# Kernel optimization log

Hardware: AMD Instinct MI355X
Metric: run time of the kernel (lower is better)

Reference implementation:

```python
import jax, jax.numpy as jnp
import numpy as np

B, N, D, H, I = 16, 1024, 1024, 16, 4096
HS = D // H  # 64
EPS = 1e-5


def setup_inputs() -> dict:
    key = jax.random.key(0)
    ks = jax.random.split(key, 8)
    w = lambda k, shape: (jax.random.normal(k, shape, jnp.float32) * 0.02)
    return {
        'hidden_states': jax.random.normal(ks[0], (B, N, D), jnp.float32),
        'ln1_g': jnp.ones((D,), jnp.float32), 'ln1_b': jnp.zeros((D,), jnp.float32),
        'ln2_g': jnp.ones((D,), jnp.float32), 'ln2_b': jnp.zeros((D,), jnp.float32),
        'wq': w(ks[1], (D, D)), 'bq': jnp.zeros((D,), jnp.float32),
        'wk': w(ks[2], (D, D)), 'bk': jnp.zeros((D,), jnp.float32),
        'wv': w(ks[3], (D, D)), 'bv': jnp.zeros((D,), jnp.float32),
        'w1': w(ks[4], (D, I)), 'b1': jnp.zeros((I,), jnp.float32),
        'w2': w(ks[5], (I, D)), 'b2': jnp.zeros((D,), jnp.float32),
    }


def _layernorm(x, g, b):
    m = jnp.mean(x, axis=-1, keepdims=True)
    v = jnp.var(x, axis=-1, keepdims=True)
    return (x - m) * jax.lax.rsqrt(v + EPS) * g + b


def _split_heads(t):
    # Faithful to transpose_for_scores: reshape (B,N,HS,H) -> (B,H,N,HS)
    # i.e. head h takes the strided feature slice t[..., h::H].
    b, n, _ = t.shape
    return t.reshape(b, n, HS, H).transpose(0, 3, 1, 2)


def _vit_layer(x, ln1_g, ln1_b, ln2_g, ln2_b, wq, bq, wk, bk, wv, bv, w1, b1, w2, b2):
    h = _layernorm(x, ln1_g, ln1_b)
    q = _split_heads(h @ wq + bq)  # [B,H,N,HS]
    k = _split_heads(h @ wk + bk)
    v = _split_heads(h @ wv + bv)
    scores = jax.nn.softmax(jnp.einsum('bhqd,bhkd->bhqk', q, k) / np.sqrt(HS).astype(np.float32), axis=-1)
    attn = jnp.einsum('bhqk,bhkd->bhqd', scores, v)          # [B,H,N,HS]
    attn = attn.transpose(0, 2, 1, 3).reshape(x.shape)       # head-major merge (as in source)
    x = x + attn
    h = _layernorm(x, ln2_g, ln2_b)
    mlp = jax.nn.silu(h @ w1 + b1) @ w2 + b2
    return x + mlp


def reference(hidden_states, ln1_g, ln1_b, ln2_g, ln2_b, wq, bq, wk, bk, wv, bv, w1, b1, w2, b2):
    return _vit_layer(hidden_states, ln1_g, ln1_b, ln2_g, ln2_b, wq, bq, wk, bk, wv, bv, w1, b1, w2, b2)
```

## Files before the change

### kernel.cpp

```cpp
#include <hip/hip_runtime.h>
#include <hip/hip_bf16.h>
#include <stdint.h>

typedef __bf16 bf16;
typedef bf16 bf16x8 __attribute__((ext_vector_type(8)));
typedef bf16 bf16x4 __attribute__((ext_vector_type(4)));
typedef float f32x4 __attribute__((ext_vector_type(4)));

static __device__ __forceinline__ f32x4 mfma16(bf16x8 a, bf16x8 b, f32x4 c) {
    return __builtin_amdgcn_mfma_f32_16x16x32_bf16(a, b, c, 0, 0, 0);
}

static __device__ __forceinline__ void gld16(const bf16* g, bf16* l) {
    __builtin_amdgcn_global_load_lds((const __attribute__((address_space(1))) void*)g,
                                     (__attribute__((address_space(3))) void*)l, 16, 0, 0);
}

static __device__ __forceinline__ uint32_t pkbf(float a, float b) {
    union { bf16 h[2]; uint32_t u; } u_;
    u_.h[0] = (bf16)a; u_.h[1] = (bf16)b;
    return u_.u;
}

template <int PERM>
__global__ __launch_bounds__(256)
void tcast_kernel(const float* __restrict__ src, bf16* __restrict__ dst, int R, int C) {
    __shared__ float t[32][33];
    const int tx = threadIdx.x, ty = threadIdx.y;
    const int c0 = blockIdx.x * 32, r0 = blockIdx.y * 32;
#pragma unroll
    for (int j = 0; j < 4; ++j)
        t[ty + j * 8][tx] = src[(size_t)(r0 + ty + j * 8) * C + c0 + tx];
    __syncthreads();
#pragma unroll
    for (int j = 0; j < 4; ++j) {
        const int c = c0 + ty + j * 8;
        const int cp = PERM ? (((c & 15) << 6) | (c >> 4)) : c;
        dst[(size_t)cp * R + r0 + tx] = (bf16)t[tx][ty + j * 8];
    }
}

__global__ __launch_bounds__(256)
void bperm_kernel(const float* __restrict__ b0, const float* __restrict__ b1,
                  const float* __restrict__ b2, float* __restrict__ dst) {
    const int i = blockIdx.x * 256 + threadIdx.x;
    const int seg = i >> 10, c = i & 1023;
    const int src = ((c & 63) << 4) | (c >> 6);
    const float* b = (seg == 0) ? b0 : (seg == 1) ? b1 : b2;
    dst[i] = b[src];
}

__global__ __launch_bounds__(256)
void ln_kernel(const float* __restrict__ x, const float* __restrict__ gg,
               const float* __restrict__ bb, bf16* __restrict__ out) {
    __shared__ float red[8];
    const int row = blockIdx.x, tid = threadIdx.x;
    const int lane = tid & 63, wid = tid >> 6;
    const float4 v = ((const float4*)(x + (size_t)row * 1024))[tid];
    float s  = v.x + v.y + v.z + v.w;
    float s2 = v.x * v.x + v.y * v.y + v.z * v.z + v.w * v.w;
#pragma unroll
    for (int m = 1; m <= 32; m <<= 1) {
        s  += __shfl_xor(s,  m);
        s2 += __shfl_xor(s2, m);
    }
    if (lane == 0) { red[wid] = s; red[wid + 4] = s2; }
    __syncthreads();
    float ts  = red[0] + red[1] + red[2] + red[3];
    float ts2 = red[4] + red[5] + red[6] + red[7];
    float mean = ts * (1.f / 1024.f);
    float var  = ts2 * (1.f / 1024.f) - mean * mean;
    float rs   = rsqrtf(var + 1e-5f);
    const float4 gv = ((const float4*)gg)[tid];
    const float4 bv = ((const float4*)bb)[tid];
    bf16x4 o;
    o[0] = (bf16)((v.x - mean) * rs * gv.x + bv.x);
    o[1] = (bf16)((v.y - mean) * rs * gv.y + bv.y);
    o[2] = (bf16)((v.z - mean) * rs * gv.z + bv.z);
    o[3] = (bf16)((v.w - mean) * rs * gv.w + bv.w);
    *(bf16x4*)(out + (size_t)row * 1024 + tid * 4) = o;
}

template <int MODE>
__global__ __launch_bounds__(256)
void gemm_bt(const bf16* __restrict__ A, const bf16* __restrict__ Bt,
             int M, int N, int K,
             const float* __restrict__ bias_a,
             const float* __restrict__ resid, float* __restrict__ outF,
             bf16* __restrict__ oQ, bf16* __restrict__ oK, bf16* __restrict__ oV,
             bf16* __restrict__ oB) {
    __shared__ alignas(16) bf16 As[3][128 * 32];
    __shared__ alignas(16) bf16 Bs[3][128 * 32];
    const int tid = threadIdx.x;
    const int wid = tid >> 6, lane = tid & 63;
    const int li = lane & 15, g = lane >> 4;

    const int nwg = gridDim.x * gridDim.y;
    const int orig = blockIdx.y * gridDim.x + blockIdx.x;
    const int wg = (orig & 7) * (nwg >> 3) + (orig >> 3);
    const int bx = wg % gridDim.x, by = wg / gridDim.x;

    const int row0 = by * 128, col0 = bx * 128;

    const int gsrc = ((tid & 3) ^ ((tid >> 3) & 3)) * 8;
    const bf16* gA0 = A + (size_t)(row0 + (tid >> 2)) * K + gsrc;
    const bf16* gA1 = A + (size_t)(row0 + 64 + (tid >> 2)) * K + gsrc;
    const bf16* gB0 = Bt + (size_t)(col0 + (tid >> 2)) * K + gsrc;
    const bf16* gB1 = Bt + (size_t)(col0 + 64 + (tid >> 2)) * K + gsrc;

    const int wr = wid >> 1, wc = wid & 1;
    f32x4 acc[4][4] = {};

    const int nt = K >> 5;
#pragma unroll
    for (int p = 0; p < 2; ++p) {
        const int kk = p << 5;
        gld16(gA0 + kk, &As[p][wid * 512]);
        gld16(gA1 + kk, &As[p][wid * 512 + 2048]);
        gld16(gB0 + kk, &Bs[p][wid * 512]);
        gld16(gB1 + kk, &Bs[p][wid * 512 + 2048]);
    }

    const int sa = (li >> 1) & 3;
    const int rdoff = (g ^ sa) * 8;

    int cur = 0;
    for (int t = 0; t < nt; ++t) {
        if (t + 2 < nt) {
            const int k2 = (t + 2) << 5;
            const int nb = (cur + 2) % 3;
            gld16(gA0 + k2, &As[nb][wid * 512]);
            gld16(gA1 + k2, &As[nb][wid * 512 + 2048]);
            gld16(gB0 + k2, &Bs[nb][wid * 512]);
            gld16(gB1 + k2, &Bs[nb][wid * 512 + 2048]);
            asm volatile("s_waitcnt vmcnt(8)" ::: "memory");
        } else if (t + 1 < nt) {
            asm volatile("s_waitcnt vmcnt(4)" ::: "memory");
        } else {
            asm volatile("s_waitcnt vmcnt(0)" ::: "memory");
        }
        __builtin_amdgcn_s_barrier();
        __builtin_amdgcn_sched_barrier(0);

        bf16x8 af[4], bg[4];
        const bf16* pa = &As[cur][(wr * 64 + li) * 32 + rdoff];
        const bf16* pb = &Bs[cur][(wc * 64 + li) * 32 + rdoff];
#pragma unroll
        for (int i = 0; i < 4; ++i) af[i] = *(const bf16x8*)(pa + i * 512);
#pragma unroll
        for (int j = 0; j < 4; ++j) bg[j] = *(const bf16x8*)(pb + j * 512);
#pragma unroll
        for (int i = 0; i < 4; ++i)
#pragma unroll
            for (int j = 0; j < 4; ++j)
                acc[i][j] = mfma16(af[i], bg[j], acc[i][j]);
        __builtin_amdgcn_sched_barrier(0);
        __builtin_amdgcn_s_barrier();
        cur = (cur + 1) % 3;
    }

    if (MODE == 0) {
        const int seg = col0 >> 10;
        const int h   = ((col0 & 1023) >> 6) + wc;
        const int bb  = row0 >> 10;
        const int n0  = (row0 & 1023) + wr * 64;
        float bias[4];
#pragma unroll
        for (int j = 0; j < 4; ++j) bias[j] = bias_a[col0 + wc * 64 + j * 16 + li];

        if (seg == 2) {
#pragma unroll
            for (int i = 0; i < 4; ++i)
#pragma unroll
                for (int j = 0; j < 4; ++j) {
                    const int d = j * 16 + li;
                    bf16x4 pv;
#pragma unroll
                    for (int r = 0; r < 4; ++r) pv[r] = (bf16)(acc[i][j][r] + bias[j]);
                    *(bf16x4*)(oV + ((size_t)(bb * 16 + h) * 64 + d) * 1024
                                   + n0 + i * 16 + g * 4) = pv;
                }
        } else {
            char* ep = (wid < 3) ? ((char*)&As[0][0] + wid * 8192)
                                 : ((char*)&Bs[0][0]);
            const float scale = (seg == 0) ? 0.125f : 1.0f;
            bf16* og = (seg == 0) ? oQ : oK;
#pragma unroll
            for (int i = 0; i < 4; ++i)
#pragma unroll
                for (int j = 0; j < 4; ++j)
#pragma unroll
                    for (int r = 0; r < 4; ++r) {
                        const int rr = i * 16 + g * 4 + r;
                        const int byte = (rr * 128 + (j * 16 + li) * 2) ^ ((rr & 7) << 4);
                        *(bf16*)(ep + byte) = (bf16)((acc[i][j][r] + bias[j]) * scale);
                    }
            bf16* gb = og + ((size_t)(bb * 16 + h) * 1024 + n0) * 64;
#pragma unroll
            for (int t = 0; t < 8; ++t) {
                const int rr = t * 8 + (lane >> 3);
                const int d0 = (lane & 7) * 8;
                const int byte = (rr * 128 + d0 * 2) ^ ((rr & 7) << 4);
                bf16x8 val = *(const bf16x8*)(ep + byte);
                *(bf16x8*)(gb + (size_t)rr * 64 + d0) = val;
            }
        }
    } else {
#pragma unroll
        for (int i = 0; i < 4; ++i) {
            const int row = row0 + wr * 64 + i * 16 + g * 4;
#pragma unroll
            for (int j = 0; j < 4; ++j) {
                const int col = col0 + wc * 64 + j * 16 + li;
                f32x4 v = acc[i][j];
                if (MODE == 1) {
                    const float bias = bias_a[col];
#pragma unroll
                    for (int r = 0; r < 4; ++r) {
                        float val = v[r] + bias;
                        val = val / (1.f + __expf(-val));
                        oB[(size_t)(row + r) * N + col] = (bf16)val;
                    }
                } else {
                    const float bias = bias_a[col];
#pragma unroll
                    for (int r = 0; r < 4; ++r) {
                        const size_t idx = (size_t)(row + r) * N + col;
                        outF[idx] = v[r] + bias + resid[idx];
                    }
                }
            }
        }
    }
}

template <int MODE>
__global__ __launch_bounds__(512, 2)
void gemm256(const bf16* __restrict__ A, const bf16* __restrict__ Bt,
             int M, int N, int K,
             const float* __restrict__ bias_a,
             const float* __restrict__ resid, float* __restrict__ outF,
             bf16* __restrict__ oB) {
    __shared__ alignas(16) bf16 As[2][256 * 64];
    __shared__ alignas(16) bf16 Bs[2][256 * 64];
    const int tid = threadIdx.x;
    const int wid = tid >> 6, lane = tid & 63;
    const int li = lane & 15, g = lane >> 4;
    const int wm = wid >> 2, wn = wid & 3;

    const int nwg = gridDim.x * gridDim.y;
    const int orig = blockIdx.y * gridDim.x + blockIdx.x;
    const int wg = (orig & 7) * (nwg >> 3) + (orig >> 3);
    const int bx = wg % gridDim.x, by = wg / gridDim.x;
    const int row0 = by * 256, col0 = bx * 256;

    const int gsrc = ((tid & 7) ^ ((tid >> 3) & 7)) << 3;
    const bf16* gA = A + (size_t)(row0 + (tid >> 3)) * K + gsrc;
    const bf16* gB = Bt + (size_t)(col0 + (tid >> 3)) * K + gsrc;

    f32x4 acc[8][4] = {};
    const int nt = K >> 6;

#pragma unroll
    for (int j = 0; j < 4; ++j) {
        gld16(gA + (size_t)(64 * j) * K, &As[0][j * 4096 + (wid << 9)]);
        gld16(gB + (size_t)(64 * j) * K, &Bs[0][j * 4096 + (wid << 9)]);
    }

    int cur = 0;
    for (int t = 0; t < nt; ++t) {
        if (t + 1 < nt) {
            const size_t koff = (size_t)(t + 1) << 6;
#pragma unroll
            for (int j = 0; j < 4; ++j) {
                gld16(gA + (size_t)(64 * j) * K + koff, &As[cur ^ 1][j * 4096 + (wid << 9)]);
                gld16(gB + (size_t)(64 * j) * K + koff, &Bs[cur ^ 1][j * 4096 + (wid << 9)]);
            }
            asm volatile("s_waitcnt vmcnt(8)" ::: "memory");
        } else {
            asm volatile("s_waitcnt vmcnt(0)" ::: "memory");
        }
        __builtin_amdgcn_s_barrier();
        __builtin_amdgcn_sched_barrier(0);

        const bf16* At = &As[cur][0];
        const bf16* Bl = &Bs[cur][0];
        bf16x8 bfr[4][2];
#pragma unroll
        for (int p = 0; p < 4; ++p) {
            bf16x8 af[2][2];
#pragma unroll
            for (int ii = 0; ii < 2; ++ii) {
                const int rr = wm * 128 + (p * 2 + ii) * 16 + li;
#pragma unroll
                for (int ks = 0; ks < 2; ++ks)
                    af[ii][ks] = *(const bf16x8*)(At + rr * 64 + (((ks * 4 + g) ^ (li & 7)) << 3));
            }
            if (p == 0) {
#pragma unroll
                for (int jf = 0; jf < 4; ++jf) {
                    const int rb = wn * 64 + jf * 16 + li;
#pragma unroll
                    for (int ks = 0; ks < 2; ++ks)
                        bfr[jf][ks] = *(const bf16x8*)(Bl + rb * 64 + (((ks * 4 + g) ^ (li & 7)) << 3));
                }
            }
            asm volatile("s_waitcnt lgkmcnt(0)" ::: "memory");
            __builtin_amdgcn_sched_barrier(0);
            __builtin_amdgcn_s_setprio(1);
#pragma unroll
            for (int ii = 0; ii < 2; ++ii)
#pragma unroll
                for (int jf = 0; jf < 4; ++jf)
#pragma unroll
                    for (int ks = 0; ks < 2; ++ks)
                        acc[p * 2 + ii][jf] = mfma16(af[ii][ks], bfr[jf][ks], acc[p * 2 + ii][jf]);
            __builtin_amdgcn_s_setprio(0);
            __builtin_amdgcn_sched_barrier(0);
            __builtin_amdgcn_s_barrier();
        }
        cur ^= 1;
    }

#pragma unroll
    for (int i = 0; i < 8; ++i) {
        const int row = row0 + wm * 128 + i * 16 + g * 4;
#pragma unroll
        for (int jf = 0; jf < 4; ++jf) {
            const int col = col0 + wn * 64 + jf * 16 + li;
            const float bias = bias_a[col];
            if (MODE == 1) {
#pragma unroll
                for (int r = 0; r < 4; ++r) {
                    float val = acc[i][jf][r] + bias;
                    val = val / (1.f + __expf(-val));
                    oB[(size_t)(row + r) * N + col] = (bf16)val;
                }
            } else {
#pragma unroll
                for (int r = 0; r < 4; ++r) {
                    const size_t idx = (size_t)(row + r) * N + col;
                    outF[idx] = acc[i][jf][r] + bias + resid[idx];
                }
            }
        }
    }
}

__global__ __launch_bounds__(256)
void attn_kernel(const bf16* __restrict__ Q, const bf16* __restrict__ Kb,
                 const bf16* __restrict__ Vt, const float* __restrict__ x,
                 float* __restrict__ out) {
    __shared__ alignas(16) bf16 Kl[2][4096];
    __shared__ alignas(16) bf16 Vl[2][4096];
    __shared__ alignas(16) char Ps[4][4096];
    const int tid = threadIdx.x, wid = tid >> 6, lane = tid & 63;
    const int li = lane & 15, g = lane >> 4;
    const int bid = blockIdx.x;
    const int bh = (bid & 7) + ((bid >> 6) << 3);
    const int qt = (bid >> 3) & 7;
    const int b = bh >> 4, h = bh & 15;
    const size_t base = (size_t)bh << 16;
    const bf16* Qp = Q + base + (size_t)(qt * 128 + wid * 32) * 64;
    const bf16* Kp = Kb + base;
    const bf16* Vp = Vt + base;
    char* psw = Ps[wid];
    const int swz = (li & 7) << 4;

    const int srow = lane >> 3;
    const int sslot = (lane & 7) ^ srow;

    bf16x8 aq[2][2];
#pragma unroll
    for (int fr = 0; fr < 2; ++fr)
#pragma unroll
        for (int ks = 0; ks < 2; ++ks)
            aq[fr][ks] = *(const bf16x8*)(Qp + (fr * 16 + li) * 64 + ks * 32 + g * 8);

#pragma unroll
    for (int hh = 0; hh < 2; ++hh) {
        const int r = wid * 16 + hh * 8 + srow;
        gld16(Kp + (size_t)r * 64 + sslot * 8, &Kl[0][(wid * 16 + hh * 8) * 64]);
        gld16(Vp + (size_t)r * 1024 + sslot * 8, &Vl[0][(wid * 16 + hh * 8) * 64]);
    }
    asm volatile("s_waitcnt vmcnt(0)" ::: "memory");
    __builtin_amdgcn_s_barrier();

    f32x4 o[2][4] = {};
    float mrun[2] = {-1e30f, -1e30f}, lrun[2] = {0.f, 0.f};

    for (int kt = 0; kt < 16; ++kt) {
        const int cur = kt & 1;
        const bf16* Kt = Kl[cur];
        const bf16* Vtl = Vl[cur];
        if (kt < 15) {
            const int nb = (kt + 1) * 64;
#pragma unroll
            for (int hh = 0; hh < 2; ++hh) {
                const int r = wid * 16 + hh * 8 + srow;
                gld16(Kp + (size_t)(nb + r) * 64 + sslot * 8,
                      &Kl[cur ^ 1][(wid * 16 + hh * 8) * 64]);
                gld16(Vp + (size_t)r * 1024 + nb + sslot * 8,
                      &Vl[cur ^ 1][(wid * 16 + hh * 8) * 64]);
            }
            asm volatile("s_waitcnt vmcnt(4)" ::: "memory");
        } else {
            asm volatile("s_waitcnt vmcnt(0)" ::: "memory");
        }
        __builtin_amdgcn_s_barrier();
        __builtin_amdgcn_sched_barrier(0);

        f32x4 s[2][4] = {};
        __builtin_amdgcn_s_setprio(1);
#pragma unroll
        for (int jc = 0; jc < 4; ++jc) {
            const int row = jc * 16 + li;
#pragma unroll
            for (int ks = 0; ks < 2; ++ks) {
                bf16x8 kf = *(const bf16x8*)(Kt + row * 64 + (((ks * 4 + g) ^ (li & 7)) * 8));
                s[0][jc] = mfma16(kf, aq[0][ks], s[0][jc]);
                s[1][jc] = mfma16(kf, aq[1][ks], s[1][jc]);
            }
        }
        __builtin_amdgcn_s_setprio(0);

#pragma unroll
        for (int fr = 0; fr < 2; ++fr) {
            float mj[4];
#pragma unroll
            for (int jc = 0; jc < 4; ++jc)
                mj[jc] = fmaxf(fmaxf(s[fr][jc][0], s[fr][jc][1]),
                               fmaxf(s[fr][jc][2], s[fr][jc][3]));
            float mx = fmaxf(fmaxf(mj[0], mj[1]), fmaxf(mj[2], mj[3]));
            mx = fmaxf(mx, __shfl_xor(mx, 16));
            mx = fmaxf(mx, __shfl_xor(mx, 32));
            if (!__all(mx <= mrun[fr] + 8.f)) {
                const float mnew = fmaxf(mrun[fr], mx);
                const float alpha = __expf(mrun[fr] - mnew);
                mrun[fr] = mnew;
                lrun[fr] *= alpha;
#pragma unroll
                for (int jd = 0; jd < 4; ++jd) o[fr][jd] *= alpha;
            }
            float pj[4];
#pragma unroll
            for (int jc = 0; jc < 4; ++jc) {
#pragma unroll
                for (int r = 0; r < 4; ++r)
                    s[fr][jc][r] = __expf(s[fr][jc][r] - mrun[fr]);
                pj[jc] = (s[fr][jc][0] + s[fr][jc][1]) + (s[fr][jc][2] + s[fr][jc][3]);
            }
            float ps = (pj[0] + pj[1]) + (pj[2] + pj[3]);
            ps += __shfl_xor(ps, 16);
            ps += __shfl_xor(ps, 32);
            lrun[fr] += ps;

            const int qb = (fr * 16 + li) * 128;
#pragma unroll
            for (int jc = 0; jc < 4; ++jc) {
                uint2 w;
                w.x = pkbf(s[fr][jc][0], s[fr][jc][1]);
                w.y = pkbf(s[fr][jc][2], s[fr][jc][3]);
                *(uint2*)(psw + ((qb + jc * 32 + g * 8) ^ swz)) = w;
            }
        }

#pragma unroll
        for (int ks2 = 0; ks2 < 2; ++ks2) {
            bf16x8 pa0 = *(const bf16x8*)(psw + ((li * 128 + ks2 * 64 + g * 16) ^ swz));
            bf16x8 pa1 = *(const bf16x8*)(psw + (((16 + li) * 128 + ks2 * 64 + g * 16) ^ swz));
            __builtin_amdgcn_s_setprio(1);
#pragma unroll
            for (int jd = 0; jd < 4; ++jd) {
                const int row = jd * 16 + li;
                bf16x8 vf = *(const bf16x8*)(Vtl + row * 64 + (((ks2 * 4 + g) ^ (li & 7)) * 8));
                o[0][jd] = mfma16(vf, pa0, o[0][jd]);
                o[1][jd] = mfma16(vf, pa1, o[1][jd]);
            }
            __builtin_amdgcn_s_setprio(0);
        }
        __builtin_amdgcn_sched_barrier(0);
        __builtin_amdgcn_s_barrier();
    }

    const int n0 = qt * 128 + wid * 32;
#pragma unroll
    for (int fr = 0; fr < 2; ++fr) {
        const float inv = 1.f / lrun[fr];
        const int n = n0 + fr * 16 + li;
        const size_t rowb = (size_t)(b * 1024 + n) * 1024 + h * 64;
#pragma unroll
        for (int jd = 0; jd < 4; ++jd) {
            const int c = jd * 16 + g * 4;
            const float4 xv = *(const float4*)(x + rowb + c);
            float4 ov;
            ov.x = xv.x + o[fr][jd][0] * inv;
            ov.y = xv.y + o[fr][jd][1] * inv;
            ov.z = xv.z + o[fr][jd][2] * inv;
            ov.w = xv.w + o[fr][jd][3] * inv;
            *(float4*)(out + rowb + c) = ov;
        }
    }
}

extern "C" void kernel_launch(void* const* d_in, const int* in_sizes, int n_in,
                              void* d_out, int out_size, void* d_ws, size_t ws_size,
                              hipStream_t stream) {
    const float* x    = (const float*)d_in[0];
    const float* ln1g = (const float*)d_in[1];
    const float* ln1b = (const float*)d_in[2];
    const float* ln2g = (const float*)d_in[3];
    const float* ln2b = (const float*)d_in[4];
    const float* wq   = (const float*)d_in[5];
    const float* bq   = (const float*)d_in[6];
    const float* wk   = (const float*)d_in[7];
    const float* bk   = (const float*)d_in[8];
    const float* wv   = (const float*)d_in[9];
    const float* bv   = (const float*)d_in[10];
    const float* w1   = (const float*)d_in[11];
    const float* b1   = (const float*)d_in[12];
    const float* w2   = (const float*)d_in[13];
    const float* b2   = (const float*)d_in[14];

    char* ws = (char*)d_ws;
    const size_t MB = 1024 * 1024;
    bf16*  Wqkvt = (bf16*)(ws);
    bf16*  W1t   = (bf16*)(ws + 6 * MB);
    bf16*  W2t   = (bf16*)(ws + 14 * MB);
    float* ares  = (float*)(ws + 22 * MB);
    bf16*  Xln   = (bf16*)(ws + 86 * MB);
    bf16*  Qb    = (bf16*)(ws + 118 * MB);
    bf16*  Kbuf  = (bf16*)(ws + 150 * MB);
    bf16*  Vtb   = (bf16*)(ws + 182 * MB);
    bf16*  mid   = (bf16*)(ws + 118 * MB);
    float* bqkvp = (float*)(ws + 245 * MB);

    dim3 tb(32, 8);
    tcast_kernel<1><<<dim3(32, 32), tb, 0, stream>>>(wq, Wqkvt,                 1024, 1024);
    tcast_kernel<1><<<dim3(32, 32), tb, 0, stream>>>(wk, Wqkvt + 1024 * 1024,   1024, 1024);
    tcast_kernel<1><<<dim3(32, 32), tb, 0, stream>>>(wv, Wqkvt + 2 * 1024 * 1024, 1024, 1024);
    tcast_kernel<0><<<dim3(128, 32), tb, 0, stream>>>(w1, W1t, 1024, 4096);
    tcast_kernel<0><<<dim3(32, 128), tb, 0, stream>>>(w2, W2t, 4096, 1024);
    bperm_kernel<<<12, 256, 0, stream>>>(bq, bk, bv, bqkvp);

    ln_kernel<<<16384, 256, 0, stream>>>(x, ln1g, ln1b, Xln);

    gemm_bt<0><<<dim3(24, 128), 256, 0, stream>>>(Xln, Wqkvt, 16384, 3072, 1024,
        bqkvp, nullptr, nullptr, Qb, Kbuf, Vtb, nullptr);

    attn_kernel<<<2048, 256, 0, stream>>>(Qb, Kbuf, Vtb, x, ares);

    ln_kernel<<<16384, 256, 0, stream>>>(ares, ln2g, ln2b, Xln);

    gemm256<1><<<dim3(16, 64), 512, 0, stream>>>(Xln, W1t, 16384, 4096, 1024,
        b1, nullptr, nullptr, mid);

    gemm256<2><<<dim3(4, 64), 512, 0, stream>>>(mid, W2t, 16384, 1024, 4096,
        b2, ares, (float*)d_out, nullptr);
}
```

Baseline: 713.3 us.

## Interleave global-to-LDS prefetch across compute phases with finer vmcnt waits

Restructures the GEMM main loop so tile loads are spread across the four compute sub-phases, prefetching parts of tiles t+1 and t+2 into the double buffer instead of issuing all loads for t+1 at the start. Fine-grained vmcnt waits and extra barriers replace the single per-iteration wait. The goal is better overlap of memory traffic with MFMA work and less stall at iteration boundaries. The cost is extra barriers and more intricate buffer-reuse ordering, which could be fragile.

```diff
diff --git a/kernel.cpp b/kernel.cpp
--- a/kernel.cpp
+++ b/kernel.cpp
@@ -257,35 +257,29 @@
     const int gsrc = ((tid & 7) ^ ((tid >> 3) & 7)) << 3;
     const bf16* gA = A + (size_t)(row0 + (tid >> 3)) * K + gsrc;
     const bf16* gB = Bt + (size_t)(col0 + (tid >> 3)) * K + gsrc;
+    const int ldst = (wid << 9);
 
     f32x4 acc[8][4] = {};
     const int nt = K >> 6;
 
-#pragma unroll
-    for (int j = 0; j < 4; ++j) {
-        gld16(gA + (size_t)(64 * j) * K, &As[0][j * 4096 + (wid << 9)]);
-        gld16(gB + (size_t)(64 * j) * K, &Bs[0][j * 4096 + (wid << 9)]);
-    }
-
-    int cur = 0;
+#define STA(tile, chunk) gld16(gA + (size_t)(64 * (chunk)) * K + ((size_t)(tile) << 6), \
+                               &As[(tile) & 1][(chunk) * 4096 + ldst])
+#define STB(tile, chunk) gld16(gB + (size_t)(64 * (chunk)) * K + ((size_t)(tile) << 6), \
+                               &Bs[(tile) & 1][(chunk) * 4096 + ldst])
+
+    STB(0, 0); STB(0, 1); STB(0, 2); STB(0, 3);
+    STA(0, 0); STA(0, 2); STA(0, 1); STA(0, 3);
+    STB(1, 0); STB(1, 1); STB(1, 2); STB(1, 3);
+    STA(1, 0); STA(1, 2);
+    asm volatile("s_waitcnt vmcnt(6)" ::: "memory");
+    __builtin_amdgcn_s_barrier();
+
     for (int t = 0; t < nt; ++t) {
-        if (t + 1 < nt) {
-            const size_t koff = (size_t)(t + 1) << 6;
-#pragma unroll
-            for (int j = 0; j < 4; ++j) {
-                gld16(gA + (size_t)(64 * j) * K + koff, &As[cur ^ 1][j * 4096 + (wid << 9)]);
-                gld16(gB + (size_t)(64 * j) * K + koff, &Bs[cur ^ 1][j * 4096 + (wid << 9)]);
-            }
-            asm volatile("s_waitcnt vmcnt(8)" ::: "memory");
-        } else {
-            asm volatile("s_waitcnt vmcnt(0)" ::: "memory");
-        }
-        __builtin_amdgcn_s_barrier();
-        __builtin_amdgcn_sched_barrier(0);
-
-        const bf16* At = &As[cur][0];
-        const bf16* Bl = &Bs[cur][0];
+        const bf16* At = &As[t & 1][0];
+        const bf16* Bl = &Bs[t & 1][0];
+        const bool s1 = (t + 1 < nt), s2 = (t + 2 < nt);
         bf16x8 bfr[4][2];
+
 #pragma unroll
         for (int p = 0; p < 4; ++p) {
             bf16x8 af[2][2];
@@ -305,6 +299,12 @@
                         bfr[jf][ks] = *(const bf16x8*)(Bl + rb * 64 + (((ks * 4 + g) ^ (li & 7)) << 3));
                 }
             }
+            if (p == 0)      { if (s1) { STA(t + 1, 1); STA(t + 1, 3); } }
+            else if (p == 1) { if (s2) { STB(t + 2, 0); STB(t + 2, 1); } }
+            else if (p == 2) { if (s2) { STB(t + 2, 2); STB(t + 2, 3); } }
+            else             { if (s2) { STA(t + 2, 0); STA(t + 2, 2); } }
+
+            __builtin_amdgcn_s_barrier();
             asm volatile("s_waitcnt lgkmcnt(0)" ::: "memory");
             __builtin_amdgcn_sched_barrier(0);
             __builtin_amdgcn_s_setprio(1);
@@ -317,10 +317,19 @@
                         acc[p * 2 + ii][jf] = mfma16(af[ii][ks], bfr[jf][ks], acc[p * 2 + ii][jf]);
             __builtin_amdgcn_s_setprio(0);
             __builtin_amdgcn_sched_barrier(0);
+            if (p == 1) {
+                if (s2) asm volatile("s_waitcnt vmcnt(10)" ::: "memory");
+                else    asm volatile("s_waitcnt vmcnt(0)" ::: "memory");
+            }
+            if (p == 3 && s1) {
+                if (s2) asm volatile("s_waitcnt vmcnt(8)" ::: "memory");
+                else    asm volatile("s_waitcnt vmcnt(0)" ::: "memory");
+            }
             __builtin_amdgcn_s_barrier();
         }
-        cur ^= 1;
-    }
+    }
+#undef STA
+#undef STB
 
 #pragma unroll
     for (int i = 0; i < 8; ++i) {
```

After: 682.3 us. 1.05x faster.
